# Kernel tuning notes

Measured on AMD Instinct MI355X. Metric: run time of the kernel, lower is better.

## Reference

```python
import jax, jax.numpy as jnp
import numpy as np

D_IN = 1024
D_OUT = 1024
NUM_HEADS = 16
HEAD_DIM = D_OUT // NUM_HEADS


def setup_inputs() -> dict:
    key = jax.random.key(0)
    ks = jax.random.split(key, 6)
    s = 0.02
    x = jax.random.normal(ks[0], (4, 2048, D_IN), dtype=jnp.float32)
    # nn.Linear weights are [out, in]
    Wq = jax.random.normal(ks[1], (D_OUT, D_IN), dtype=jnp.float32) * s
    Wk = jax.random.normal(ks[2], (D_OUT, D_IN), dtype=jnp.float32) * s
    Wv = jax.random.normal(ks[3], (D_OUT, D_IN), dtype=jnp.float32) * s
    Wo = jax.random.normal(ks[4], (D_OUT, D_OUT), dtype=jnp.float32) * s
    bo = jax.random.normal(ks[5], (D_OUT,), dtype=jnp.float32) * s
    return {"x": x, "Wq": Wq, "Wk": Wk, "Wv": Wv, "Wo": Wo, "bo": bo}


def reference(x, Wq, Wk, Wv, Wo, bo):
    B, T, _ = x.shape
    # project and split heads: [B, H, T, hd]
    def proj(W):
        return (x @ W.T).reshape(B, T, NUM_HEADS, HEAD_DIM).transpose(0, 2, 1, 3)
    q, k, v = proj(Wq), proj(Wk), proj(Wv)
    scores = jnp.einsum('bhqd,bhkd->bhqk', q, k) / jnp.sqrt(jnp.float32(HEAD_DIM))
    causal = jnp.tril(jnp.ones((T, T), dtype=bool))  # True = keep
    scores = jnp.where(causal, scores, -jnp.inf)
    attn = jax.nn.softmax(scores, axis=-1)
    ctx = jnp.einsum('bhqk,bhkd->bhqd', attn, v)  # [B,H,T,hd]
    ctx = ctx.transpose(0, 2, 1, 3).reshape(B, T, D_OUT)
    return ctx @ Wo.T + bo
```

## Files before the change

### kernel.cpp

```cpp
#include <hip/hip_runtime.h>

#define NH 16
#define HD 64
#define TSEQ 2048
#define DMODEL 1024

typedef __attribute__((ext_vector_type(8))) short short8;
typedef __attribute__((ext_vector_type(4))) float f32x4;

static __device__ __forceinline__ unsigned short f2bf(float f) {
    unsigned u = __builtin_bit_cast(unsigned, f);
    u += 0x7FFF + ((u >> 16) & 1);
    return (unsigned short)(u >> 16);
}

static __device__ __forceinline__ unsigned cvtpk(float a, float b) {
    unsigned r;
    asm("v_cvt_pk_bf16_f32 %0, %1, %2" : "=v"(r) : "v"(a), "v"(b));
    return r;
}

__global__ __launch_bounds__(256) void cast_f32_bf16(const float* __restrict__ src,
                                                     unsigned short* __restrict__ dst, int n4) {
    int i = blockIdx.x * 256 + threadIdx.x;
    if (i >= n4) return;
    float4 v = reinterpret_cast<const float4*>(src)[i];
    ushort4 o;
    o.x = f2bf(v.x); o.y = f2bf(v.y); o.z = f2bf(v.z); o.w = f2bf(v.w);
    reinterpret_cast<ushort4*>(dst)[i] = o;
}

__global__ __launch_bounds__(256) void cast_weights(const float* __restrict__ Wq,
                                                    const float* __restrict__ Wk,
                                                    const float* __restrict__ Wv,
                                                    const float* __restrict__ Wo,
                                                    unsigned short* __restrict__ dq,
                                                    unsigned short* __restrict__ dk,
                                                    unsigned short* __restrict__ dv,
                                                    unsigned short* __restrict__ dwo) {
    int g = blockIdx.x >> 10;
    int i = (blockIdx.x & 1023) * 256 + threadIdx.x;
    const float* s = (g == 0) ? Wq : (g == 1) ? Wk : (g == 2) ? Wv : Wo;
    unsigned short* d = (g == 0) ? dq : (g == 1) ? dk : (g == 2) ? dv : dwo;
    float4 v = reinterpret_cast<const float4*>(s)[i];
    ushort4 o;
    o.x = f2bf(v.x); o.y = f2bf(v.y); o.z = f2bf(v.z); o.w = f2bf(v.w);
    reinterpret_cast<ushort4*>(d)[i] = o;
}

static __device__ __forceinline__ void gemm256_mainloop(
    const unsigned short* __restrict__ A, const unsigned short* __restrict__ Bt,
    int m0, int n0, unsigned short* As, unsigned short* Bs, f32x4 acc[4][4]) {
    const int tid = threadIdx.x, lane = tid & 63, w = tid >> 6;
    const int wr = w >> 1, wc = w & 1;
    const int lg = lane >> 4, ll = lane & 15;
    const int strow = tid >> 2;
    const int su = tid & 3;
    const int rx = ll & 3;

    const f32x4 zero = {0.f, 0.f, 0.f, 0.f};
#pragma unroll
    for (int i = 0; i < 4; i++)
#pragma unroll
        for (int j = 0; j < 4; j++) acc[i][j] = zero;

    auto stage = [&](int kt, int slot) {
#pragma unroll
        for (int s = 0; s < 2; ++s) {
            int row = s * 128 + strow;
            int gcol = kt * 32 + ((su ^ (row & 3)) * 8);
            __builtin_amdgcn_global_load_lds(
                (const __attribute__((address_space(1))) void*)(A + (size_t)(m0 + row) * DMODEL + gcol),
                (__attribute__((address_space(3))) void*)(As + slot * 8192 + row * 32 + su * 8), 16, 0, 0);
        }
        {
            int row = strow;
            int gcol = kt * 32 + ((su ^ (row & 3)) * 8);
            __builtin_amdgcn_global_load_lds(
                (const __attribute__((address_space(1))) void*)(Bt + (size_t)(n0 + row) * DMODEL + gcol),
                (__attribute__((address_space(3))) void*)(Bs + slot * 4096 + row * 32 + su * 8), 16, 0, 0);
        }
    };

    stage(0, 0);
    stage(1, 1);
    asm volatile("s_waitcnt vmcnt(3)" ::: "memory");
    __builtin_amdgcn_s_barrier();
    __builtin_amdgcn_sched_barrier(0);

    int pb = 0;
#pragma unroll 1
    for (int kt = 0; kt < 32; ++kt) {
        short8 af[4], bf[4];
#pragma unroll
        for (int i = 0; i < 4; i++)
            af[i] = *(const short8*)(As + pb * 8192 + (wr * 64 + i * 16 + ll) * 32 + ((lg ^ rx) * 8));
#pragma unroll
        for (int j = 0; j < 4; j++)
            bf[j] = *(const short8*)(Bs + pb * 4096 + (wc * 64 + j * 16 + ll) * 32 + ((lg ^ rx) * 8));
        const int pn = (pb + 2 >= 3) ? (pb - 1) : (pb + 2);
        if (kt + 2 < 32) stage(kt + 2, pn);

        asm volatile("s_waitcnt lgkmcnt(0)" ::: "memory");
        __builtin_amdgcn_sched_barrier(0);
        __builtin_amdgcn_s_setprio(1);
#pragma unroll
        for (int i = 0; i < 4; i++)
#pragma unroll
            for (int j = 0; j < 4; j++)
                acc[i][j] = __builtin_amdgcn_mfma_f32_16x16x32_bf16(af[i], bf[j], acc[i][j], 0, 0, 0);
        __builtin_amdgcn_s_setprio(0);
        __builtin_amdgcn_sched_barrier(0);
        if (kt + 2 < 32) {
            asm volatile("s_waitcnt vmcnt(3)" ::: "memory");
        } else {
            asm volatile("s_waitcnt vmcnt(0)" ::: "memory");
        }
        __builtin_amdgcn_s_barrier();
        __builtin_amdgcn_sched_barrier(0);
        pb = (pb + 1 >= 3) ? 0 : (pb + 1);
    }
}

#define QSCALE 0.180336880f
__global__ __launch_bounds__(512) void gemm_qkv(const unsigned short* __restrict__ xb,
                                                const unsigned short* __restrict__ Wqb,
                                                const unsigned short* __restrict__ Wkb,
                                                const unsigned short* __restrict__ Wvb,
                                                unsigned short* __restrict__ Q,
                                                unsigned short* __restrict__ K,
                                                unsigned short* __restrict__ Vt) {
    __shared__ __attribute__((aligned(16))) unsigned short As[3 * 256 * 32];
    __shared__ __attribute__((aligned(16))) unsigned short Bs[3 * 128 * 32];
    const int m0 = blockIdx.x * 256;
    const int n0 = blockIdx.y * 128;
    const int z = blockIdx.z;
    const unsigned short* Bt = (z == 0) ? Wqb : ((z == 1) ? Wkb : Wvb);
    unsigned short* out = (z == 0) ? Q : ((z == 1) ? K : Vt);

    f32x4 acc[4][4];
    gemm256_mainloop(xb, Bt, m0, n0, As, Bs, acc);

    const int lane = threadIdx.x & 63, w = threadIdx.x >> 6;
    const int wr = w >> 1, wc = w & 1;
    const int lg = lane >> 4, ll = lane & 15;
    const float sc = (z == 0) ? QSCALE : 1.0f;
    if (z == 2) {
#pragma unroll
        for (int i = 0; i < 4; i++)
#pragma unroll
            for (int j = 0; j < 4; j++) {
                int row0 = m0 + wr * 64 + i * 16 + lg * 4;
                int col = n0 + wc * 64 + j * 16 + ll;
                int b = row0 >> 11, t0 = row0 & 2047;
                int h = col >> 6, d = col & 63;
                ushort4 v4;
                v4.x = f2bf(acc[i][j][0]); v4.y = f2bf(acc[i][j][1]);
                v4.z = f2bf(acc[i][j][2]); v4.w = f2bf(acc[i][j][3]);
                *(ushort4*)&Vt[(((size_t)(b * NH + h)) * HD + d) * TSEQ + t0] = v4;
            }
    } else {
#pragma unroll
        for (int i = 0; i < 4; i++)
#pragma unroll
            for (int j = 0; j < 4; j++)
#pragma unroll
                for (int r = 0; r < 4; r++) {
                    int row = m0 + wr * 64 + i * 16 + lg * 4 + r;
                    int col = n0 + wc * 64 + j * 16 + ll;
                    int b = row >> 11, t = row & 2047;
                    int h = col >> 6, d = col & 63;
                    out[(((size_t)(b * NH + h)) * TSEQ + t) * HD + d] = f2bf(acc[i][j][r] * sc);
                }
    }
}

__global__ __launch_bounds__(512) void gemm_out(const unsigned short* __restrict__ ctx,
                                                const unsigned short* __restrict__ Wob,
                                                const float* __restrict__ bo,
                                                float* __restrict__ out) {
    __shared__ __attribute__((aligned(16))) unsigned short As[3 * 256 * 32];
    __shared__ __attribute__((aligned(16))) unsigned short Bs[3 * 128 * 32];
    const int m0 = blockIdx.x * 256;
    const int n0 = blockIdx.y * 128;

    f32x4 acc[4][4];
    gemm256_mainloop(ctx, Wob, m0, n0, As, Bs, acc);

    const int lane = threadIdx.x & 63, w = threadIdx.x >> 6;
    const int wr = w >> 1, wc = w & 1;
    const int lg = lane >> 4, ll = lane & 15;
#pragma unroll
    for (int i = 0; i < 4; i++)
#pragma unroll
        for (int j = 0; j < 4; j++) {
            int col = n0 + wc * 64 + j * 16 + ll;
            float bias = bo[col];
#pragma unroll
            for (int r = 0; r < 4; r++) {
                int row = m0 + wr * 64 + i * 16 + lg * 4 + r;
                out[(size_t)row * DMODEL + col] = acc[i][j][r] + bias;
            }
        }
}

__global__ __launch_bounds__(512) void attn(const unsigned short* __restrict__ Qg,
                                            const unsigned short* __restrict__ Kg,
                                            const unsigned short* __restrict__ Vg,
                                            unsigned short* __restrict__ ctx) {
    __shared__ __attribute__((aligned(16))) unsigned short Ks[64][68];
    __shared__ __attribute__((aligned(16))) unsigned short Vs[64][68];
    __shared__ __attribute__((aligned(16))) unsigned short Pl[256][72];

    const int tid = threadIdx.x, lane = tid & 63, w = tid >> 6;
    const int wq = w * 32;
    const int lg = lane >> 4;
    const int ll = lane & 15;
    const int bh = blockIdx.x;
    const int q0 = (gridDim.y - 1 - blockIdx.y) * 256;
    const unsigned short* Qh = Qg + (size_t)bh * TSEQ * HD;
    const unsigned short* Kh = Kg + (size_t)bh * TSEQ * HD;
    const unsigned short* Vh = Vg + (size_t)bh * HD * TSEQ;

    short8 qf[2][2];
#pragma unroll
    for (int rb = 0; rb < 2; rb++)
#pragma unroll
        for (int ks = 0; ks < 2; ks++)
            qf[rb][ks] = *(const short8*)(Qh + (size_t)(q0 + wq + rb * 16 + ll) * HD + ks * 32 + lg * 8);

    float mrun[2] = {-1e30f, -1e30f}, lrun[2] = {0.f, 0.f};
    const f32x4 zerov = {0.f, 0.f, 0.f, 0.f};
    f32x4 o_t[2][4];
#pragma unroll
    for (int rb = 0; rb < 2; rb++)
#pragma unroll
        for (int db = 0; db < 4; db++) o_t[rb][db] = zerov;

    const int sr = tid >> 3;
    const int sc = (tid & 7) * 8;
    short8 kreg, vreg;
    kreg = *(const short8*)(Kh + (size_t)sr * HD + sc);
    vreg = *(const short8*)(Vh + (size_t)sr * TSEQ + sc);

    const int nkv = q0 / 64 + 4;
    for (int kt = 0; kt < nkv; kt++) {
        const int kv0 = kt * 64;
        __builtin_amdgcn_s_barrier();
        __builtin_amdgcn_sched_barrier(0);
        *(short8*)&Ks[sr][sc] = kreg;
        *(short8*)&Vs[sr][sc] = vreg;
        if (kt + 1 < nkv) {
            const int nv0 = kv0 + 64;
            kreg = *(const short8*)(Kh + (size_t)(nv0 + sr) * HD + sc);
            vreg = *(const short8*)(Vh + (size_t)sr * TSEQ + nv0 + sc);
        }
        __builtin_amdgcn_sched_barrier(0);
        asm volatile("s_waitcnt lgkmcnt(0)" ::: "memory");
        __builtin_amdgcn_s_barrier();
        __builtin_amdgcn_sched_barrier(0);

        if (kv0 > q0 + wq + 31) continue;

        short8 af0[4], af1[4];
#pragma unroll
        for (int cb = 0; cb < 4; cb++) {
            af0[cb] = *(const short8*)&Ks[cb * 16 + ll][lg * 8];
            af1[cb] = *(const short8*)&Ks[cb * 16 + ll][32 + lg * 8];
        }
        f32x4 st[2][4];
#pragma unroll
        for (int rb = 0; rb < 2; rb++)
#pragma unroll
            for (int cb = 0; cb < 4; cb++)
                st[rb][cb] = __builtin_amdgcn_mfma_f32_16x16x32_bf16(af0[cb], qf[rb][0], zerov, 0, 0, 0);
#pragma unroll
        for (int rb = 0; rb < 2; rb++)
#pragma unroll
            for (int cb = 0; cb < 4; cb++)
                st[rb][cb] = __builtin_amdgcn_mfma_f32_16x16x32_bf16(af1[cb], qf[rb][1], st[rb][cb], 0, 0, 0);

        if (kv0 + 63 > q0 + wq) {
#pragma unroll
            for (int rb = 0; rb < 2; rb++)
#pragma unroll
                for (int cb = 0; cb < 4; cb++)
#pragma unroll
                    for (int r = 0; r < 4; r++) {
                        int kvl = cb * 16 + lg * 4 + r;
                        int ql = wq + rb * 16 + ll;
                        if (kv0 + kvl > q0 + ql) st[rb][cb][r] = -1e30f;
                    }
        }

        float mx[2];
#pragma unroll
        for (int rb = 0; rb < 2; rb++) {
            float a0 = fmaxf(fmaxf(st[rb][0][0], st[rb][0][1]), fmaxf(st[rb][0][2], st[rb][0][3]));
            float a1 = fmaxf(fmaxf(st[rb][1][0], st[rb][1][1]), fmaxf(st[rb][1][2], st[rb][1][3]));
            float a2 = fmaxf(fmaxf(st[rb][2][0], st[rb][2][1]), fmaxf(st[rb][2][2], st[rb][2][3]));
            float a3 = fmaxf(fmaxf(st[rb][3][0], st[rb][3][1]), fmaxf(st[rb][3][2], st[rb][3][3]));
            float m = fmaxf(fmaxf(a0, a1), fmaxf(a2, a3));
            m = fmaxf(m, __shfl_xor(m, 16));
            m = fmaxf(m, __shfl_xor(m, 32));
            mx[rb] = m;
        }
        float need = fmaxf(mx[0] - mrun[0], mx[1] - mrun[1]);
        if (__any(need > 8.f)) {
#pragma unroll
            for (int rb = 0; rb < 2; rb++) {
                float mold = mrun[rb];
                float mn = fmaxf(mold, mx[rb]);
                float rs = __builtin_amdgcn_exp2f(mold - mn);
                mrun[rb] = mn;
                lrun[rb] *= rs;
#pragma unroll
                for (int db = 0; db < 4; db++)
#pragma unroll
                    for (int r = 0; r < 4; r++) o_t[rb][db][r] *= rs;
            }
        }
#pragma unroll
        for (int rb = 0; rb < 2; rb++) {
            float sum = 0.f;
#pragma unroll
            for (int cb = 0; cb < 4; cb++) {
                float p0 = __builtin_amdgcn_exp2f(st[rb][cb][0] - mrun[rb]);
                float p1 = __builtin_amdgcn_exp2f(st[rb][cb][1] - mrun[rb]);
                float p2 = __builtin_amdgcn_exp2f(st[rb][cb][2] - mrun[rb]);
                float p3 = __builtin_amdgcn_exp2f(st[rb][cb][3] - mrun[rb]);
                sum += (p0 + p1) + (p2 + p3);
                uint2 pw;
                pw.x = cvtpk(p0, p1);
                pw.y = cvtpk(p2, p3);
                *(uint2*)&Pl[wq + rb * 16 + ll][cb * 16 + lg * 4] = pw;
            }
            sum += __shfl_xor(sum, 16);
            sum += __shfl_xor(sum, 32);
            lrun[rb] += sum;
        }
        asm volatile("s_waitcnt lgkmcnt(0)" ::: "memory");
        __builtin_amdgcn_sched_barrier(0);

#pragma unroll
        for (int ks = 0; ks < 2; ks++) {
            short8 pa[2], va[4];
#pragma unroll
            for (int rb = 0; rb < 2; rb++)
                pa[rb] = *(const short8*)&Pl[wq + rb * 16 + ll][ks * 32 + lg * 8];
#pragma unroll
            for (int db = 0; db < 4; db++)
                va[db] = *(const short8*)&Vs[db * 16 + ll][ks * 32 + lg * 8];
#pragma unroll
            for (int rb = 0; rb < 2; rb++)
#pragma unroll
                for (int db = 0; db < 4; db++)
                    o_t[rb][db] = __builtin_amdgcn_mfma_f32_16x16x32_bf16(va[db], pa[rb], o_t[rb][db], 0, 0, 0);
        }
    }

    const int b = bh >> 4, h = bh & 15;
#pragma unroll
    for (int rb = 0; rb < 2; rb++) {
        float linv = 1.f / lrun[rb];
#pragma unroll
        for (int db = 0; db < 4; db++) {
            uint2 pw;
            pw.x = cvtpk(o_t[rb][db][0] * linv, o_t[rb][db][1] * linv);
            pw.y = cvtpk(o_t[rb][db][2] * linv, o_t[rb][db][3] * linv);
            *(uint2*)&Pl[wq + rb * 16 + ll][db * 16 + lg * 4] = pw;
        }
    }
    asm volatile("s_waitcnt lgkmcnt(0)" ::: "memory");
    __builtin_amdgcn_sched_barrier(0);
#pragma unroll
    for (int rb = 0; rb < 2; rb++)
#pragma unroll
        for (int half = 0; half < 2; half++) {
            short8 v = *(const short8*)&Pl[wq + rb * 16 + ll][half * 32 + lg * 8];
            size_t row = (size_t)(b * TSEQ + q0 + wq + rb * 16 + ll);
            *(short8*)(ctx + (row * NH + h) * HD + half * 32 + lg * 8) = v;
        }
}

extern "C" void kernel_launch(void* const* d_in, const int* in_sizes, int n_in,
                              void* d_out, int out_size, void* d_ws, size_t ws_size,
                              hipStream_t stream) {
    const float* x  = (const float*)d_in[0];
    const float* Wq = (const float*)d_in[1];
    const float* Wk = (const float*)d_in[2];
    const float* Wv = (const float*)d_in[3];
    const float* Wo = (const float*)d_in[4];
    const float* bo = (const float*)d_in[5];
    float* out = (float*)d_out;

    char* ws = (char*)d_ws;
    unsigned short* xb   = (unsigned short*)(ws);
    unsigned short* Wqb  = (unsigned short*)(ws + 16777216);
    unsigned short* Wkb  = (unsigned short*)(ws + 18874368);
    unsigned short* Wvb  = (unsigned short*)(ws + 20971520);
    unsigned short* Wob  = (unsigned short*)(ws + 23068672);
    unsigned short* Qb   = (unsigned short*)(ws + 25165824);
    unsigned short* Kb   = (unsigned short*)(ws + 41943040);
    unsigned short* Vtb  = (unsigned short*)(ws + 58720256);
    unsigned short* ctxb = (unsigned short*)(ws + 75497472);

    cast_f32_bf16<<<8192, 256, 0, stream>>>(x, xb, 2097152);
    cast_weights<<<4096, 256, 0, stream>>>(Wq, Wk, Wv, Wo, Wqb, Wkb, Wvb, Wob);

    gemm_qkv<<<dim3(32, 8, 3), 512, 0, stream>>>(xb, Wqb, Wkb, Wvb, Qb, Kb, Vtb);
    attn<<<dim3(64, 8), 512, 0, stream>>>(Qb, Kb, Vtb, ctxb);
    gemm_out<<<dim3(32, 8), 512, 0, stream>>>(ctxb, Wob, bo, out);
}
```

Measured before the change: 170.8 us.

## Double-buffer K/V tiles in LDS and use one barrier per iteration

The attention kernel's K and V shared-memory tiles become two buffers. Each iteration computes from the current buffer, then stores the prefetched next tile into the other buffer and issues global loads for the tile after that. This drops one of the two block barriers per KV step and lets the LDS write of the next tile sit after compute instead of before it. The cost is twice the K/V LDS footprint, which may lower occupancy, and the global prefetch now has a full iteration of latency to hide.

```diff
diff --git a/kernel.cpp b/kernel.cpp
--- a/kernel.cpp
+++ b/kernel.cpp
@@ -208,8 +208,8 @@
                                             const unsigned short* __restrict__ Kg,
                                             const unsigned short* __restrict__ Vg,
                                             unsigned short* __restrict__ ctx) {
-    __shared__ __attribute__((aligned(16))) unsigned short Ks[64][68];
-    __shared__ __attribute__((aligned(16))) unsigned short Vs[64][68];
+    __shared__ __attribute__((aligned(16))) unsigned short Ks[2][64][68];
+    __shared__ __attribute__((aligned(16))) unsigned short Vs[2][64][68];
     __shared__ __attribute__((aligned(16))) unsigned short Pl[256][72];
 
     const int tid = threadIdx.x, lane = tid & 63, w = tid >> 6;
@@ -239,124 +239,134 @@
 
     const int sr = tid >> 3;
     const int sc = (tid & 7) * 8;
-    short8 kreg, vreg;
-    kreg = *(const short8*)(Kh + (size_t)sr * HD + sc);
-    vreg = *(const short8*)(Vh + (size_t)sr * TSEQ + sc);
-
     const int nkv = q0 / 64 + 4;
+
+    short8 kreg = *(const short8*)(Kh + (size_t)sr * HD + sc);
+    short8 vreg = *(const short8*)(Vh + (size_t)sr * TSEQ + sc);
+    *(short8*)&Ks[0][sr][sc] = kreg;
+    *(short8*)&Vs[0][sr][sc] = vreg;
+    if (nkv > 1) {
+        kreg = *(const short8*)(Kh + (size_t)(64 + sr) * HD + sc);
+        vreg = *(const short8*)(Vh + (size_t)sr * TSEQ + 64 + sc);
+    }
+    asm volatile("s_waitcnt lgkmcnt(0)" ::: "memory");
+    __builtin_amdgcn_s_barrier();
+    __builtin_amdgcn_sched_barrier(0);
+
     for (int kt = 0; kt < nkv; kt++) {
         const int kv0 = kt * 64;
-        __builtin_amdgcn_s_barrier();
-        __builtin_amdgcn_sched_barrier(0);
-        *(short8*)&Ks[sr][sc] = kreg;
-        *(short8*)&Vs[sr][sc] = vreg;
+        const int cur = kt & 1;
+
+        if (kv0 <= q0 + wq + 31) {
+            short8 af0[4], af1[4];
+#pragma unroll
+            for (int cb = 0; cb < 4; cb++) {
+                af0[cb] = *(const short8*)&Ks[cur][cb * 16 + ll][lg * 8];
+                af1[cb] = *(const short8*)&Ks[cur][cb * 16 + ll][32 + lg * 8];
+            }
+            f32x4 st[2][4];
+#pragma unroll
+            for (int rb = 0; rb < 2; rb++)
+#pragma unroll
+                for (int cb = 0; cb < 4; cb++)
+                    st[rb][cb] = __builtin_amdgcn_mfma_f32_16x16x32_bf16(af0[cb], qf[rb][0], zerov, 0, 0, 0);
+#pragma unroll
+            for (int rb = 0; rb < 2; rb++)
+#pragma unroll
+                for (int cb = 0; cb < 4; cb++)
+                    st[rb][cb] = __builtin_amdgcn_mfma_f32_16x16x32_bf16(af1[cb], qf[rb][1], st[rb][cb], 0, 0, 0);
+
+            if (kv0 + 63 > q0 + wq) {
+#pragma unroll
+                for (int rb = 0; rb < 2; rb++)
+#pragma unroll
+                    for (int cb = 0; cb < 4; cb++)
+#pragma unroll
+                        for (int r = 0; r < 4; r++) {
+                            int kvl = cb * 16 + lg * 4 + r;
+                            int ql = wq + rb * 16 + ll;
+                            if (kv0 + kvl > q0 + ql) st[rb][cb][r] = -1e30f;
+                        }
+            }
+
+            float mx[2];
+#pragma unroll
+            for (int rb = 0; rb < 2; rb++) {
+                float a0 = fmaxf(fmaxf(st[rb][0][0], st[rb][0][1]), fmaxf(st[rb][0][2], st[rb][0][3]));
+                float a1 = fmaxf(fmaxf(st[rb][1][0], st[rb][1][1]), fmaxf(st[rb][1][2], st[rb][1][3]));
+                float a2 = fmaxf(fmaxf(st[rb][2][0], st[rb][2][1]), fmaxf(st[rb][2][2], st[rb][2][3]));
+                float a3 = fmaxf(fmaxf(st[rb][3][0], st[rb][3][1]), fmaxf(st[rb][3][2], st[rb][3][3]));
+                float m = fmaxf(fmaxf(a0, a1), fmaxf(a2, a3));
+                m = fmaxf(m, __shfl_xor(m, 16));
+                m = fmaxf(m, __shfl_xor(m, 32));
+                mx[rb] = m;
+            }
+            float need = fmaxf(mx[0] - mrun[0], mx[1] - mrun[1]);
+            if (__any(need > 8.f)) {
+#pragma unroll
+                for (int rb = 0; rb < 2; rb++) {
+                    float mold = mrun[rb];
+                    float mn = fmaxf(mold, mx[rb]);
+                    float rs = __builtin_amdgcn_exp2f(mold - mn);
+                    mrun[rb] = mn;
+                    lrun[rb] *= rs;
+#pragma unroll
+                    for (int db = 0; db < 4; db++)
+#pragma unroll
+                        for (int r = 0; r < 4; r++) o_t[rb][db][r] *= rs;
+                }
+            }
+#pragma unroll
+            for (int rb = 0; rb < 2; rb++) {
+                float sum = 0.f;
+#pragma unroll
+                for (int cb = 0; cb < 4; cb++) {
+                    float p0 = __builtin_amdgcn_exp2f(st[rb][cb][0] - mrun[rb]);
+                    float p1 = __builtin_amdgcn_exp2f(st[rb][cb][1] - mrun[rb]);
+                    float p2 = __builtin_amdgcn_exp2f(st[rb][cb][2] - mrun[rb]);
+                    float p3 = __builtin_amdgcn_exp2f(st[rb][cb][3] - mrun[rb]);
+                    sum += (p0 + p1) + (p2 + p3);
+                    uint2 pw;
+                    pw.x = cvtpk(p0, p1);
+                    pw.y = cvtpk(p2, p3);
+                    *(uint2*)&Pl[wq + rb * 16 + ll][cb * 16 + lg * 4] = pw;
+                }
+                sum += __shfl_xor(sum, 16);
+                sum += __shfl_xor(sum, 32);
+                lrun[rb] += sum;
+            }
+            asm volatile("s_waitcnt lgkmcnt(0)" ::: "memory");
+            __builtin_amdgcn_sched_barrier(0);
+
+#pragma unroll
+            for (int ks = 0; ks < 2; ks++) {
+                short8 pa[2], va[4];
+#pragma unroll
+                for (int rb = 0; rb < 2; rb++)
+                    pa[rb] = *(const short8*)&Pl[wq + rb * 16 + ll][ks * 32 + lg * 8];
+#pragma unroll
+                for (int db = 0; db < 4; db++)
+                    va[db] = *(const short8*)&Vs[cur][db * 16 + ll][ks * 32 + lg * 8];
+#pragma unroll
+                for (int rb = 0; rb < 2; rb++)
+#pragma unroll
+                    for (int db = 0; db < 4; db++)
+                        o_t[rb][db] = __builtin_amdgcn_mfma_f32_16x16x32_bf16(va[db], pa[rb], o_t[rb][db], 0, 0, 0);
+            }
+        }
+
         if (kt + 1 < nkv) {
-            const int nv0 = kv0 + 64;
-            kreg = *(const short8*)(Kh + (size_t)(nv0 + sr) * HD + sc);
-            vreg = *(const short8*)(Vh + (size_t)sr * TSEQ + nv0 + sc);
-        }
-        __builtin_amdgcn_sched_barrier(0);
+            *(short8*)&Ks[cur ^ 1][sr][sc] = kreg;
+            *(short8*)&Vs[cur ^ 1][sr][sc] = vreg;
+            if (kt + 2 < nkv) {
+                const int nv0 = (kt + 2) * 64;
+                kreg = *(const short8*)(Kh + (size_t)(nv0 + sr) * HD + sc);
+                vreg = *(const short8*)(Vh + (size_t)sr * TSEQ + nv0 + sc);
+            }
+        }
         asm volatile("s_waitcnt lgkmcnt(0)" ::: "memory");
         __builtin_amdgcn_s_barrier();
         __builtin_amdgcn_sched_barrier(0);
-
-        if (kv0 > q0 + wq + 31) continue;
-
-        short8 af0[4], af1[4];
-#pragma unroll
-        for (int cb = 0; cb < 4; cb++) {
-            af0[cb] = *(const short8*)&Ks[cb * 16 + ll][lg * 8];
-            af1[cb] = *(const short8*)&Ks[cb * 16 + ll][32 + lg * 8];
-        }
-        f32x4 st[2][4];
-#pragma unroll
-        for (int rb = 0; rb < 2; rb++)
-#pragma unroll
-            for (int cb = 0; cb < 4; cb++)
-                st[rb][cb] = __builtin_amdgcn_mfma_f32_16x16x32_bf16(af0[cb], qf[rb][0], zerov, 0, 0, 0);
-#pragma unroll
-        for (int rb = 0; rb < 2; rb++)
-#pragma unroll
-            for (int cb = 0; cb < 4; cb++)
-                st[rb][cb] = __builtin_amdgcn_mfma_f32_16x16x32_bf16(af1[cb], qf[rb][1], st[rb][cb], 0, 0, 0);
-
-        if (kv0 + 63 > q0 + wq) {
-#pragma unroll
-            for (int rb = 0; rb < 2; rb++)
-#pragma unroll
-                for (int cb = 0; cb < 4; cb++)
-#pragma unroll
-                    for (int r = 0; r < 4; r++) {
-                        int kvl = cb * 16 + lg * 4 + r;
-                        int ql = wq + rb * 16 + ll;
-                        if (kv0 + kvl > q0 + ql) st[rb][cb][r] = -1e30f;
-                    }
-        }
-
-        float mx[2];
-#pragma unroll
-        for (int rb = 0; rb < 2; rb++) {
-            float a0 = fmaxf(fmaxf(st[rb][0][0], st[rb][0][1]), fmaxf(st[rb][0][2], st[rb][0][3]));
-            float a1 = fmaxf(fmaxf(st[rb][1][0], st[rb][1][1]), fmaxf(st[rb][1][2], st[rb][1][3]));
-            float a2 = fmaxf(fmaxf(st[rb][2][0], st[rb][2][1]), fmaxf(st[rb][2][2], st[rb][2][3]));
-            float a3 = fmaxf(fmaxf(st[rb][3][0], st[rb][3][1]), fmaxf(st[rb][3][2], st[rb][3][3]));
-            float m = fmaxf(fmaxf(a0, a1), fmaxf(a2, a3));
-            m = fmaxf(m, __shfl_xor(m, 16));
-            m = fmaxf(m, __shfl_xor(m, 32));
-            mx[rb] = m;
-        }
-        float need = fmaxf(mx[0] - mrun[0], mx[1] - mrun[1]);
-        if (__any(need > 8.f)) {
-#pragma unroll
-            for (int rb = 0; rb < 2; rb++) {
-                float mold = mrun[rb];
-                float mn = fmaxf(mold, mx[rb]);
-                float rs = __builtin_amdgcn_exp2f(mold - mn);
-                mrun[rb] = mn;
-                lrun[rb] *= rs;
-#pragma unroll
-                for (int db = 0; db < 4; db++)
-#pragma unroll
-                    for (int r = 0; r < 4; r++) o_t[rb][db][r] *= rs;
-            }
-        }
-#pragma unroll
-        for (int rb = 0; rb < 2; rb++) {
-            float sum = 0.f;
-#pragma unroll
-            for (int cb = 0; cb < 4; cb++) {
-                float p0 = __builtin_amdgcn_exp2f(st[rb][cb][0] - mrun[rb]);
-                float p1 = __builtin_amdgcn_exp2f(st[rb][cb][1] - mrun[rb]);
-                float p2 = __builtin_amdgcn_exp2f(st[rb][cb][2] - mrun[rb]);
-                float p3 = __builtin_amdgcn_exp2f(st[rb][cb][3] - mrun[rb]);
-                sum += (p0 + p1) + (p2 + p3);
-                uint2 pw;
-                pw.x = cvtpk(p0, p1);
-                pw.y = cvtpk(p2, p3);
-                *(uint2*)&Pl[wq + rb * 16 + ll][cb * 16 + lg * 4] = pw;
-            }
-            sum += __shfl_xor(sum, 16);
-            sum += __shfl_xor(sum, 32);
-            lrun[rb] += sum;
-        }
-        asm volatile("s_waitcnt lgkmcnt(0)" ::: "memory");
-        __builtin_amdgcn_sched_barrier(0);
-
-#pragma unroll
-        for (int ks = 0; ks < 2; ks++) {
-            short8 pa[2], va[4];
-#pragma unroll
-            for (int rb = 0; rb < 2; rb++)
-                pa[rb] = *(const short8*)&Pl[wq + rb * 16 + ll][ks * 32 + lg * 8];
-#pragma unroll
-            for (int db = 0; db < 4; db++)
-                va[db] = *(const short8*)&Vs[db * 16 + ll][ks * 32 + lg * 8];
-#pragma unroll
-            for (int rb = 0; rb < 2; rb++)
-#pragma unroll
-                for (int db = 0; db < 4; db++)
-                    o_t[rb][db] = __builtin_amdgcn_mfma_f32_16x16x32_bf16(va[db], pa[rb], o_t[rb][db], 0, 0, 0);
-        }
     }
 
     const int b = bh >> 4, h = bh & 15;
```

Result: slower. 174.9 us (+2.4%).
